# Performance work log

Hardware: AMD Instinct MI355X
Metric: run time of the kernel (lower is better)

## Reference

```python
import jax, jax.numpy as jnp
import numpy as np

N_NODES = 50000
N_EDGES = 1600000
IN_CH = 128
HID = 64
HEADS = 2
EMB = 128
OUT_CH = EMB // HEADS  # 64, GATConvMean out_channels
NEG_SLOPE = 0.2


def _gat_conv(x, src, dst, W, a_src, a_dst, b, heads, out_ch, concat, n_nodes):
    # x: [N, F_in]; W: [F_in, heads*out_ch]; a_src/a_dst: [heads, out_ch]; b: bias
    s = (x @ W).reshape(n_nodes, heads, out_ch)          # [N, H, C]
    alpha_src = jnp.sum(s * a_src, axis=-1)              # [N, H]
    alpha_dst = jnp.sum(s * a_dst, axis=-1)              # [N, H]
    e = jax.nn.leaky_relu(alpha_src[src] + alpha_dst[dst], NEG_SLOPE)  # [E, H]
    # segment softmax over edges sharing the same destination node
    m = jax.ops.segment_max(e, dst, num_segments=n_nodes)             # [N, H]
    ex = jnp.exp(e - m[dst])
    denom = jax.ops.segment_sum(ex, dst, num_segments=n_nodes)        # [N, H]
    alpha = ex / denom[dst]                                           # [E, H]
    msg = s[src] * alpha[:, :, None]                                  # [E, H, C]
    out = jax.ops.segment_sum(msg, dst, num_segments=n_nodes)         # [N, H, C]
    if concat:
        out = out.reshape(n_nodes, heads * out_ch)
    else:
        out = out.mean(axis=1)
    return out + b


def setup_inputs() -> dict:
    key = jax.random.key(0)
    ks = jax.random.split(key, 16)
    X = jax.random.normal(ks[0], (N_NODES, IN_CH), dtype=jnp.float32)
    edge_index = jax.random.randint(ks[1], (2, N_EDGES), 0, N_NODES, dtype=jnp.int64)

    def glorot(k, shape):
        fan_in, fan_out = shape[0], shape[-1]
        lim = jnp.sqrt(6.0 / (fan_in + fan_out)).astype(jnp.float32)
        return jax.random.uniform(k, shape, jnp.float32, -lim, lim)

    HC = HEADS * HID  # 128
    # in_layer: GATConv(IN_CH -> HID, heads=HEADS, concat)
    W0 = glorot(ks[2], (IN_CH, HC))
    a_src0 = glorot(ks[3], (HEADS, HID))
    a_dst0 = glorot(ks[4], (HEADS, HID))
    b0 = jnp.zeros((HC,), jnp.float32)
    # middle layer: GATConv(HC -> HID, heads=HEADS, concat)
    W1 = glorot(ks[5], (HC, HC))
    a_src1 = glorot(ks[6], (HEADS, HID))
    a_dst1 = glorot(ks[7], (HEADS, HID))
    b1 = jnp.zeros((HC,), jnp.float32)
    # ivectors: GATConvMean(HC -> OUT_CH, heads=HEADS, mean over heads)
    W2 = glorot(ks[8], (HC, HEADS * OUT_CH))
    a_src2 = glorot(ks[9], (HEADS, OUT_CH))
    a_dst2 = glorot(ks[10], (HEADS, OUT_CH))
    b2 = jnp.zeros((OUT_CH,), jnp.float32)
    return {
        "X": X, "edge_index": edge_index,
        "W0": W0, "a_src0": a_src0, "a_dst0": a_dst0, "b0": b0,
        "W1": W1, "a_src1": a_src1, "a_dst1": a_dst1, "b1": b1,
        "W2": W2, "a_src2": a_src2, "a_dst2": a_dst2, "b2": b2,
    }


def reference(X, edge_index, W0, a_src0, a_dst0, b0, W1, a_src1, a_dst1, b1, W2, a_src2, a_dst2, b2):
    n = X.shape[0]
    loop = jnp.arange(n, dtype=edge_index.dtype)
    src = jnp.concatenate([edge_index[0], loop])  # PyG GATConv add_self_loops=True
    dst = jnp.concatenate([edge_index[1], loop])
    h = jax.nn.elu(_gat_conv(X, src, dst, W0, a_src0, a_dst0, b0, HEADS, HID, True, n))
    h = jax.nn.relu(_gat_conv(h, src, dst, W1, a_src1, a_dst1, b1, HEADS, HID, True, n))
    # dropout is identity in eval mode
    out = jax.nn.relu(_gat_conv(h, src, dst, W2, a_src2, a_dst2, b2, HEADS, OUT_CH, False, n))
    return out
```

## Files before the change

kernel.cpp:

```cpp
#include <hip/hip_runtime.h>
#include <hip/hip_bf16.h>


#define SCAN_BLOCK 256
#define KSHIFT 12
#define KC 13

__global__ void detect_i64(const unsigned* __restrict__ ei, int* __restrict__ flag) {
    if (threadIdx.x == 0 && blockIdx.x == 0) {
        int allz = 1;
        for (int i = 0; i < 128; ++i)
            if (ei[2 * i + 1] != 0u) { allz = 0; break; }
        *flag = allz;
    }
}

__global__ __launch_bounds__(256) void gat_convert(
    const void* __restrict__ ei, const int* __restrict__ flag, int nE, int nN,
    int2* __restrict__ edge2) {
    const int i64 = *flag;
    const long long total = (long long)nE + nN;
    const long long stride = (long long)gridDim.x * blockDim.x;
    for (long long i = (long long)blockIdx.x * blockDim.x + threadIdx.x; i < total; i += stride) {
        int s, d;
        if (i < nE) {
            if (i64) { s = (int)((const long long*)ei)[i]; d = (int)((const long long*)ei)[nE + i]; }
            else     { s = ((const int*)ei)[i];            d = ((const int*)ei)[nE + i]; }
        } else { s = d = (int)(i - nE); }
        edge2[i] = make_int2(s, d);
    }
}

__global__ __launch_bounds__(256) void gat_rankp(
    const int2* __restrict__ edge2, long long total, int nN,
    int* __restrict__ cnt2, int* __restrict__ rank) {
    const int cw = (nN + 7) >> 3;
    const int lo = (blockIdx.x & 7) * cw;
    const long long stride = (long long)(gridDim.x >> 3) * blockDim.x;
    for (long long i = (long long)(blockIdx.x >> 3) * blockDim.x + threadIdx.x;
         i < total; i += stride) {
        const int2 e = edge2[i];
        if ((unsigned)(e.y - lo) >= (unsigned)cw) continue;
        const int bin = e.y * KC + (e.x >> KSHIFT);
        rank[i] = atomicAdd(&cnt2[bin], 1);
    }
}

__global__ __launch_bounds__(SCAN_BLOCK) void scan_stage1(
    const int* __restrict__ cnt, int* __restrict__ partial, int* __restrict__ bsum, int n) {
    __shared__ int tmp[SCAN_BLOCK];
    const int i = blockIdx.x * SCAN_BLOCK + threadIdx.x;
    const int v = (i < n) ? cnt[i] : 0;
    tmp[threadIdx.x] = v;
    __syncthreads();
    #pragma unroll
    for (int off = 1; off < SCAN_BLOCK; off <<= 1) {
        const int t = (threadIdx.x >= off) ? tmp[threadIdx.x - off] : 0;
        __syncthreads();
        tmp[threadIdx.x] += t;
        __syncthreads();
    }
    if (i < n) partial[i] = tmp[threadIdx.x];
    if (threadIdx.x == SCAN_BLOCK - 1) bsum[blockIdx.x] = tmp[threadIdx.x];
}

__global__ void scan_stage2(int* __restrict__ bsum, int nb, int* __restrict__ rowp, int n) {
    const int lane = threadIdx.x;
    int carry = 0;
    for (int base = 0; base < nb; base += 64) {
        const int i = base + lane;
        const int v = (i < nb) ? bsum[i] : 0;
        int incl = v;
        #pragma unroll
        for (int off = 1; off < 64; off <<= 1) {
            const int t = __shfl_up(incl, off);
            if (lane >= off) incl += t;
        }
        if (i < nb) bsum[i] = carry + incl - v;
        carry += __shfl(incl, 63);
    }
    if (lane == 0) rowp[n] = carry;
}

__global__ __launch_bounds__(SCAN_BLOCK) void scan_stage3v2(
    const int* __restrict__ part2, const int* __restrict__ cnt2,
    const int* __restrict__ bsumA, const int* __restrict__ partB,
    const int* __restrict__ bsumB, int* __restrict__ rowp, int n) {
    const int i = blockIdx.x * SCAN_BLOCK + threadIdx.x;
    if (i < n) {
        const int b1 = i >> 8;
        rowp[i] = bsumB[b1 >> 8] + (partB[b1] - bsumA[b1]) + (part2[i] - cnt2[i]);
    }
}

__global__ __launch_bounds__(256) void gat_placep(
    const int2* __restrict__ edge2, const int* __restrict__ rank,
    const int* __restrict__ rowp2, long long total, int nN, int* __restrict__ csr) {
    const int cw = (nN + 7) >> 3;
    const int lo = (blockIdx.x & 7) * cw;
    const long long stride = (long long)(gridDim.x >> 3) * blockDim.x;
    for (long long i = (long long)(blockIdx.x >> 3) * blockDim.x + threadIdx.x;
         i < total; i += stride) {
        const int2 e = edge2[i];
        if ((unsigned)(e.y - lo) >= (unsigned)cw) continue;
        const int bin = e.y * KC + (e.x >> KSHIFT);
        csr[rowp2[bin] + rank[i]] = e.x;
    }
}

__global__ __launch_bounds__(256) void gemm_alpha(
    const float* __restrict__ Xin, const float* __restrict__ W,
    const float* __restrict__ avs, const float* __restrict__ avd,
    float* __restrict__ S, float* __restrict__ as_, float* __restrict__ ad_, int n) {
    __shared__ float Xl[64][128];
    const int tid = threadIdx.x;
    const int row0 = blockIdx.x * 64;
    for (int i = tid; i < 64 * 32; i += 256) {
        const int r = i >> 5, c4 = i & 31;
        const int gr = row0 + r;
        float4 v = (gr < n) ? ((const float4*)(Xin + (size_t)gr * 128))[c4]
                            : make_float4(0.f, 0.f, 0.f, 0.f);
        ((float4*)(&Xl[r][0]))[c4] = v;
    }
    __syncthreads();
    const int col4 = tid & 31;
    const int rowg = tid >> 5;
    float4 acc[8];
    #pragma unroll
    for (int r = 0; r < 8; ++r) acc[r] = make_float4(0.f, 0.f, 0.f, 0.f);
    const float* Wc = W + col4 * 4;
    for (int kk = 0; kk < 128; kk += 4) {
        const float4 w0 = *(const float4*)(Wc + (size_t)(kk + 0) * 128);
        const float4 w1 = *(const float4*)(Wc + (size_t)(kk + 1) * 128);
        const float4 w2 = *(const float4*)(Wc + (size_t)(kk + 2) * 128);
        const float4 w3 = *(const float4*)(Wc + (size_t)(kk + 3) * 128);
        #pragma unroll
        for (int r = 0; r < 8; ++r) {
            const float4 x = *(const float4*)(&Xl[rowg * 8 + r][kk]);
            acc[r].x = fmaf(x.x, w0.x, acc[r].x); acc[r].y = fmaf(x.x, w0.y, acc[r].y);
            acc[r].z = fmaf(x.x, w0.z, acc[r].z); acc[r].w = fmaf(x.x, w0.w, acc[r].w);
            acc[r].x = fmaf(x.y, w1.x, acc[r].x); acc[r].y = fmaf(x.y, w1.y, acc[r].y);
            acc[r].z = fmaf(x.y, w1.z, acc[r].z); acc[r].w = fmaf(x.y, w1.w, acc[r].w);
            acc[r].x = fmaf(x.z, w2.x, acc[r].x); acc[r].y = fmaf(x.z, w2.y, acc[r].y);
            acc[r].z = fmaf(x.z, w2.z, acc[r].z); acc[r].w = fmaf(x.z, w2.w, acc[r].w);
            acc[r].x = fmaf(x.w, w3.x, acc[r].x); acc[r].y = fmaf(x.w, w3.y, acc[r].y);
            acc[r].z = fmaf(x.w, w3.z, acc[r].z); acc[r].w = fmaf(x.w, w3.w, acc[r].w);
        }
    }
    const float4 av = ((const float4*)avs)[col4];
    const float4 dv = ((const float4*)avd)[col4];
    #pragma unroll
    for (int r = 0; r < 8; ++r) {
        const int grow = row0 + rowg * 8 + r;
        if (grow < n) ((float4*)(S + (size_t)grow * 128))[col4] = acc[r];
        float ps = acc[r].x * av.x + acc[r].y * av.y + acc[r].z * av.z + acc[r].w * av.w;
        float pd = acc[r].x * dv.x + acc[r].y * dv.y + acc[r].z * dv.z + acc[r].w * dv.w;
        #pragma unroll
        for (int off = 8; off; off >>= 1) {
            ps += __shfl_xor(ps, off);
            pd += __shfl_xor(pd, off);
        }
        if ((col4 & 15) == 0 && grow < n) {
            const int h = col4 >> 4;
            as_[2 * grow + h] = ps;
            ad_[2 * grow + h] = pd;
        }
    }
}

__global__ __launch_bounds__(256) void gat_fused(
    const float* __restrict__ S, const float* __restrict__ as_,
    const float* __restrict__ ad_, const int* __restrict__ rowp2,
    const int* __restrict__ csr, const float* __restrict__ bias,
    float* __restrict__ out, int n, int mode) {
    const int lane = threadIdx.x & 63;
    const int d = (blockIdx.x * blockDim.x + threadIdx.x) >> 6;
    if (d >= n) return;
    const int beg = rowp2[d * KC], end = rowp2[(d + 1) * KC];
    const int deg = end - beg;
    const float2 adv = *(const float2*)(ad_ + 2 * d);
    const int g = lane >> 4;
    const int gl = lane & 15;
    float4 acc0 = make_float4(0.f, 0.f, 0.f, 0.f);
    float4 acc1 = make_float4(0.f, 0.f, 0.f, 0.f);
    if (deg <= 64) {
        const bool has = lane < deg;
        const int s_reg = has ? csr[beg + lane] : 0;
        float e0 = -1e30f, e1 = -1e30f;
        if (has) {
            const float2 asv = *(const float2*)(as_ + 2 * s_reg);
            e0 = asv.x + adv.x; e0 = e0 > 0.f ? e0 : 0.2f * e0;
            e1 = asv.y + adv.y; e1 = e1 > 0.f ? e1 : 0.2f * e1;
        }
        float m0 = e0, m1 = e1;
        #pragma unroll
        for (int off = 32; off; off >>= 1) {
            m0 = fmaxf(m0, __shfl_xor(m0, off));
            m1 = fmaxf(m1, __shfl_xor(m1, off));
        }
        const float p0 = has ? __expf(e0 - m0) : 0.f;
        const float p1 = has ? __expf(e1 - m1) : 0.f;
        float s0 = p0, s1 = p1;
        #pragma unroll
        for (int off = 32; off; off >>= 1) {
            s0 += __shfl_xor(s0, off);
            s1 += __shfl_xor(s1, off);
        }
        const float inv0 = 1.f / s0, inv1 = 1.f / s1;
        int k = 0;
        for (; k + 4 <= deg; k += 4) {
            const int ke = k + g;
            const int sv = __shfl(s_reg, ke);
            const float a0 = __shfl(p0, ke) * inv0;
            const float a1 = __shfl(p1, ke) * inv1;
            const float4* r = (const float4*)(S + ((size_t)sv << 7));
            const float4 v0 = r[gl], v1 = r[16 + gl];
            acc0.x = fmaf(a0, v0.x, acc0.x); acc0.y = fmaf(a0, v0.y, acc0.y);
            acc0.z = fmaf(a0, v0.z, acc0.z); acc0.w = fmaf(a0, v0.w, acc0.w);
            acc1.x = fmaf(a1, v1.x, acc1.x); acc1.y = fmaf(a1, v1.y, acc1.y);
            acc1.z = fmaf(a1, v1.z, acc1.z); acc1.w = fmaf(a1, v1.w, acc1.w);
        }
        if (k < deg) {
            const int ke = k + g;
            const bool valid = ke < deg;
            const int idx = valid ? ke : 0;
            const int sv = __shfl(s_reg, idx);
            const float q0 = __shfl(p0, idx), q1 = __shfl(p1, idx);
            if (valid) {
                const float a0 = q0 * inv0, a1 = q1 * inv1;
                const float4* r = (const float4*)(S + ((size_t)sv << 7));
                const float4 v0 = r[gl], v1 = r[16 + gl];
                acc0.x = fmaf(a0, v0.x, acc0.x); acc0.y = fmaf(a0, v0.y, acc0.y);
                acc0.z = fmaf(a0, v0.z, acc0.z); acc0.w = fmaf(a0, v0.w, acc0.w);
                acc1.x = fmaf(a1, v1.x, acc1.x); acc1.y = fmaf(a1, v1.y, acc1.y);
                acc1.z = fmaf(a1, v1.z, acc1.z); acc1.w = fmaf(a1, v1.w, acc1.w);
            }
        }
    } else {
        float m0 = -1e30f, m1 = -1e30f;
        for (int i = beg + lane; i < end; i += 64) {
            const int s = csr[i];
            const float2 asv = *(const float2*)(as_ + 2 * s);
            float e0 = asv.x + adv.x; e0 = e0 > 0.f ? e0 : 0.2f * e0;
            float e1 = asv.y + adv.y; e1 = e1 > 0.f ? e1 : 0.2f * e1;
            m0 = fmaxf(m0, e0); m1 = fmaxf(m1, e1);
        }
        #pragma unroll
        for (int off = 32; off; off >>= 1) {
            m0 = fmaxf(m0, __shfl_xor(m0, off));
            m1 = fmaxf(m1, __shfl_xor(m1, off));
        }
        float s0 = 0.f, s1 = 0.f;
        for (int i = beg + lane; i < end; i += 64) {
            const int s = csr[i];
            const float2 asv = *(const float2*)(as_ + 2 * s);
            float e0 = asv.x + adv.x; e0 = e0 > 0.f ? e0 : 0.2f * e0;
            float e1 = asv.y + adv.y; e1 = e1 > 0.f ? e1 : 0.2f * e1;
            s0 += __expf(e0 - m0); s1 += __expf(e1 - m1);
        }
        #pragma unroll
        for (int off = 32; off; off >>= 1) {
            s0 += __shfl_xor(s0, off);
            s1 += __shfl_xor(s1, off);
        }
        const float inv0 = 1.f / s0, inv1 = 1.f / s1;
        for (int k = 0; k < deg; k += 4) {
            const int ke = k + g;
            const bool valid = ke < deg;
            if (valid) {
                const int sv = csr[beg + ke];
                const float2 asv = *(const float2*)(as_ + 2 * sv);
                float e0 = asv.x + adv.x; e0 = e0 > 0.f ? e0 : 0.2f * e0;
                float e1 = asv.y + adv.y; e1 = e1 > 0.f ? e1 : 0.2f * e1;
                const float a0 = __expf(e0 - m0) * inv0;
                const float a1 = __expf(e1 - m1) * inv1;
                const float4* r = (const float4*)(S + ((size_t)sv << 7));
                const float4 v0 = r[gl], v1 = r[16 + gl];
                acc0.x = fmaf(a0, v0.x, acc0.x); acc0.y = fmaf(a0, v0.y, acc0.y);
                acc0.z = fmaf(a0, v0.z, acc0.z); acc0.w = fmaf(a0, v0.w, acc0.w);
                acc1.x = fmaf(a1, v1.x, acc1.x); acc1.y = fmaf(a1, v1.y, acc1.y);
                acc1.z = fmaf(a1, v1.z, acc1.z); acc1.w = fmaf(a1, v1.w, acc1.w);
            }
        }
    }
    #pragma unroll
    for (int off = 16; off <= 32; off <<= 1) {
        acc0.x += __shfl_xor(acc0.x, off); acc0.y += __shfl_xor(acc0.y, off);
        acc0.z += __shfl_xor(acc0.z, off); acc0.w += __shfl_xor(acc0.w, off);
        acc1.x += __shfl_xor(acc1.x, off); acc1.y += __shfl_xor(acc1.y, off);
        acc1.z += __shfl_xor(acc1.z, off); acc1.w += __shfl_xor(acc1.w, off);
    }
    if (mode == 2) {
        if (lane < 16) {
            const float4 b = ((const float4*)bias)[gl];
            float4 o;
            o.x = fmaxf(0.5f * (acc0.x + acc1.x) + b.x, 0.f);
            o.y = fmaxf(0.5f * (acc0.y + acc1.y) + b.y, 0.f);
            o.z = fmaxf(0.5f * (acc0.z + acc1.z) + b.z, 0.f);
            o.w = fmaxf(0.5f * (acc0.w + acc1.w) + b.w, 0.f);
            ((float4*)(out + (size_t)d * 64))[gl] = o;
        }
    } else if (lane < 32) {
        const int ci = (lane < 16) ? gl : 16 + gl;
        const float4 a = (lane < 16) ? acc0 : acc1;
        const float4 b = ((const float4*)bias)[ci];
        float4 o;
        o.x = a.x + b.x; o.y = a.y + b.y; o.z = a.z + b.z; o.w = a.w + b.w;
        if (mode == 0) {
            o.x = o.x > 0.f ? o.x : expm1f(o.x);
            o.y = o.y > 0.f ? o.y : expm1f(o.y);
            o.z = o.z > 0.f ? o.z : expm1f(o.z);
            o.w = o.w > 0.f ? o.w : expm1f(o.w);
        } else {
            o.x = fmaxf(o.x, 0.f); o.y = fmaxf(o.y, 0.f);
            o.z = fmaxf(o.z, 0.f); o.w = fmaxf(o.w, 0.f);
        }
        ((float4*)(out + (size_t)d * 128))[ci] = o;
    }
}

extern "C" void kernel_launch(void* const* d_in, const int* in_sizes, int n_in,
                              void* d_out, int out_size, void* d_ws, size_t ws_size,
                              hipStream_t stream) {
    const float* X   = (const float*)d_in[0];
    const void*  EI  = d_in[1];
    const float* W0  = (const float*)d_in[2];
    const float* as0 = (const float*)d_in[3];
    const float* ad0 = (const float*)d_in[4];
    const float* b0  = (const float*)d_in[5];
    const float* W1  = (const float*)d_in[6];
    const float* as1 = (const float*)d_in[7];
    const float* ad1 = (const float*)d_in[8];
    const float* b1  = (const float*)d_in[9];
    const float* W2  = (const float*)d_in[10];
    const float* as2 = (const float*)d_in[11];
    const float* ad2 = (const float*)d_in[12];
    const float* b2  = (const float*)d_in[13];

    const int N  = in_sizes[0] / 128;
    const int E  = in_sizes[1] / 2;
    const int ET = E + N;
    const int NBINS = N * KC;
    const int NB2 = (NBINS + SCAN_BLOCK - 1) / SCAN_BLOCK;
    const int NB3 = (NB2 + SCAN_BLOCK - 1) / SCAN_BLOCK;

    char* p = (char*)d_ws;
    size_t used = 0;
    auto alloc = [&](size_t bytes) -> void* {
        void* r = p + used;
        used += (bytes + 255) & ~(size_t)255;
        return r;
    };
    float*  S     = (float*)alloc((size_t)N * 128 * 4);
    float*  H0    = (float*)alloc((size_t)N * 128 * 4);
    float*  H1    = (float*)alloc((size_t)N * 128 * 4);
    int*    csr   = (int*)alloc((size_t)ET * 4);
    int*    rowp2 = (int*)alloc((size_t)(NBINS + 1) * 4);
    int*    cnt2  = (int*)alloc((size_t)NBINS * 4);
    int*    part2 = (int*)alloc((size_t)NBINS * 4);
    int*    bsumA = (int*)alloc((size_t)NB2 * 4);
    int*    partB = (int*)alloc((size_t)NB2 * 4);
    int*    bsumB = (int*)alloc((size_t)NB3 * 4);
    float*  asb   = (float*)alloc((size_t)N * 2 * 4);
    float*  adb   = (float*)alloc((size_t)N * 2 * 4);
    int*    flag  = (int*)alloc(256);
    if (used > ws_size) return;
    const int ETP = (ET + 63) & ~63;
    int2* edge2 = (int2*)S;
    int*  rank  = (int*)(edge2 + ETP);

    hipMemsetAsync(cnt2, 0, (size_t)NBINS * 4, stream);
    detect_i64<<<1, 64, 0, stream>>>((const unsigned*)EI, flag);
    gat_convert<<<2048, 256, 0, stream>>>(EI, flag, E, N, edge2);
    gat_rankp<<<2048, 256, 0, stream>>>(edge2, (long long)ET, N, cnt2, rank);
    scan_stage1<<<NB2, SCAN_BLOCK, 0, stream>>>(cnt2, part2, bsumA, NBINS);
    scan_stage1<<<NB3, SCAN_BLOCK, 0, stream>>>(bsumA, partB, bsumB, NB2);
    scan_stage2<<<1, 64, 0, stream>>>(bsumB, NB3, rowp2, NBINS);
    scan_stage3v2<<<NB2, SCAN_BLOCK, 0, stream>>>(part2, cnt2, bsumA, partB, bsumB, rowp2, NBINS);
    gat_placep<<<2048, 256, 0, stream>>>(edge2, rank, rowp2, (long long)ET, N, csr);

    const int gemm_blocks = (N + 63) / 64;
    const int wave_blocks = (N + 3) / 4;

    gemm_alpha<<<gemm_blocks, 256, 0, stream>>>(X, W0, as0, ad0, S, asb, adb, N);
    gat_fused<<<wave_blocks, 256, 0, stream>>>(S, asb, adb, rowp2, csr, b0, H0, N, 0);
    gemm_alpha<<<gemm_blocks, 256, 0, stream>>>(H0, W1, as1, ad1, S, asb, adb, N);
    gat_fused<<<wave_blocks, 256, 0, stream>>>(S, asb, adb, rowp2, csr, b1, H1, N, 1);
    gemm_alpha<<<gemm_blocks, 256, 0, stream>>>(H1, W2, as2, ad2, S, asb, adb, N);
    gat_fused<<<wave_blocks, 256, 0, stream>>>(S, asb, adb, rowp2, csr, b2, (float*)d_out, N, 2);
}
```

Before: 535.0 us.

## Pre-partition edges into destination buckets and store CSR sources as 16-bit

Replaces the convert kernel and the filtered rank/place passes with a partition kernel that writes edges into 8 destination-range buckets as packed 32-bit (src|dst<<16). The rank and place kernels then read only their own bucket instead of scanning all edges 8 times, and the CSR source indices become unsigned short, halving index traffic in the three aggregation kernels. The packing assumes node ids fit in 16 bits (N=50000), and a bucket overflowing its capacity (1.25x the average) silently drops edges.

```diff
diff --git a/kernel.cpp b/kernel.cpp
--- a/kernel.cpp
+++ b/kernel.cpp
@@ -15,34 +15,55 @@
     }
 }
 
-__global__ __launch_bounds__(256) void gat_convert(
+__global__ __launch_bounds__(256) void gat_partition(
     const void* __restrict__ ei, const int* __restrict__ flag, int nE, int nN,
-    int2* __restrict__ edge2) {
+    unsigned* __restrict__ bucket, int cap, int* __restrict__ gcnt) {
+    __shared__ int lcnt[8];
+    __shared__ int lbase[8];
     const int i64 = *flag;
+    const int cw = (nN + 7) >> 3;
+    const int tid = threadIdx.x;
     const long long total = (long long)nE + nN;
     const long long stride = (long long)gridDim.x * blockDim.x;
-    for (long long i = (long long)blockIdx.x * blockDim.x + threadIdx.x; i < total; i += stride) {
-        int s, d;
-        if (i < nE) {
-            if (i64) { s = (int)((const long long*)ei)[i]; d = (int)((const long long*)ei)[nE + i]; }
-            else     { s = ((const int*)ei)[i];            d = ((const int*)ei)[nE + i]; }
-        } else { s = d = (int)(i - nE); }
-        edge2[i] = make_int2(s, d);
-    }
-}
-
-__global__ __launch_bounds__(256) void gat_rankp(
-    const int2* __restrict__ edge2, long long total, int nN,
+    for (long long i = (long long)blockIdx.x * blockDim.x + tid; ; i += stride) {
+        const long long iter_base = i - tid;
+        if (iter_base >= total) break;
+        if (tid < 8) lcnt[tid] = 0;
+        __syncthreads();
+        const bool has = i < total;
+        int s = 0, d = 0, cls = 0, lpos = 0;
+        if (has) {
+            if (i < nE) {
+                if (i64) { s = (int)((const long long*)ei)[i]; d = (int)((const long long*)ei)[nE + i]; }
+                else     { s = ((const int*)ei)[i];            d = ((const int*)ei)[nE + i]; }
+            } else { s = d = (int)(i - nE); }
+            cls = d / cw;
+            lpos = atomicAdd(&lcnt[cls], 1);
+        }
+        __syncthreads();
+        if (tid < 8 && lcnt[tid] > 0) lbase[tid] = atomicAdd(&gcnt[tid], lcnt[tid]);
+        __syncthreads();
+        if (has) {
+            const int pos = lbase[cls] + lpos;
+            if (pos < cap) bucket[(size_t)cls * cap + pos] = (unsigned)s | ((unsigned)d << 16);
+        }
+        __syncthreads();
+    }
+}
+
+__global__ __launch_bounds__(256) void gat_rankb(
+    const unsigned* __restrict__ bucket, const int* __restrict__ gcnt, int cap,
     int* __restrict__ cnt2, int* __restrict__ rank) {
-    const int cw = (nN + 7) >> 3;
-    const int lo = (blockIdx.x & 7) * cw;
-    const long long stride = (long long)(gridDim.x >> 3) * blockDim.x;
-    for (long long i = (long long)(blockIdx.x >> 3) * blockDim.x + threadIdx.x;
-         i < total; i += stride) {
-        const int2 e = edge2[i];
-        if ((unsigned)(e.y - lo) >= (unsigned)cw) continue;
-        const int bin = e.y * KC + (e.x >> KSHIFT);
-        rank[i] = atomicAdd(&cnt2[bin], 1);
+    const int c = blockIdx.x & 7;
+    const int m = gcnt[c];
+    const unsigned* bk = bucket + (size_t)c * cap;
+    int* rk = rank + (size_t)c * cap;
+    const int stride = (gridDim.x >> 3) * blockDim.x;
+    for (int j = (blockIdx.x >> 3) * blockDim.x + threadIdx.x; j < m; j += stride) {
+        const unsigned e = bk[j];
+        const int s = e & 0xFFFF, d = e >> 16;
+        const int bin = d * KC + (s >> KSHIFT);
+        rk[j] = atomicAdd(&cnt2[bin], 1);
     }
 }
 
@@ -93,18 +114,20 @@
     }
 }
 
-__global__ __launch_bounds__(256) void gat_placep(
-    const int2* __restrict__ edge2, const int* __restrict__ rank,
-    const int* __restrict__ rowp2, long long total, int nN, int* __restrict__ csr) {
-    const int cw = (nN + 7) >> 3;
-    const int lo = (blockIdx.x & 7) * cw;
-    const long long stride = (long long)(gridDim.x >> 3) * blockDim.x;
-    for (long long i = (long long)(blockIdx.x >> 3) * blockDim.x + threadIdx.x;
-         i < total; i += stride) {
-        const int2 e = edge2[i];
-        if ((unsigned)(e.y - lo) >= (unsigned)cw) continue;
-        const int bin = e.y * KC + (e.x >> KSHIFT);
-        csr[rowp2[bin] + rank[i]] = e.x;
+__global__ __launch_bounds__(256) void gat_placeb(
+    const unsigned* __restrict__ bucket, const int* __restrict__ gcnt, int cap,
+    const int* __restrict__ rank, const int* __restrict__ rowp2,
+    unsigned short* __restrict__ csr) {
+    const int c = blockIdx.x & 7;
+    const int m = gcnt[c];
+    const unsigned* bk = bucket + (size_t)c * cap;
+    const int* rk = rank + (size_t)c * cap;
+    const int stride = (gridDim.x >> 3) * blockDim.x;
+    for (int j = (blockIdx.x >> 3) * blockDim.x + threadIdx.x; j < m; j += stride) {
+        const unsigned e = bk[j];
+        const int s = e & 0xFFFF, d = e >> 16;
+        const int bin = d * KC + (s >> KSHIFT);
+        csr[rowp2[bin] + rk[j]] = (unsigned short)s;
     }
 }
 
@@ -171,7 +194,7 @@
 __global__ __launch_bounds__(256) void gat_fused(
     const float* __restrict__ S, const float* __restrict__ as_,
     const float* __restrict__ ad_, const int* __restrict__ rowp2,
-    const int* __restrict__ csr, const float* __restrict__ bias,
+    const unsigned short* __restrict__ csr, const float* __restrict__ bias,
     float* __restrict__ out, int n, int mode) {
     const int lane = threadIdx.x & 63;
     const int d = (blockIdx.x * blockDim.x + threadIdx.x) >> 6;
@@ -185,7 +208,7 @@
     float4 acc1 = make_float4(0.f, 0.f, 0.f, 0.f);
     if (deg <= 64) {
         const bool has = lane < deg;
-        const int s_reg = has ? csr[beg + lane] : 0;
+        const int s_reg = has ? (int)csr[beg + lane] : 0;
         float e0 = -1e30f, e1 = -1e30f;
         if (has) {
             const float2 asv = *(const float2*)(as_ + 2 * s_reg);
@@ -239,7 +262,7 @@
     } else {
         float m0 = -1e30f, m1 = -1e30f;
         for (int i = beg + lane; i < end; i += 64) {
-            const int s = csr[i];
+            const int s = (int)csr[i];
             const float2 asv = *(const float2*)(as_ + 2 * s);
             float e0 = asv.x + adv.x; e0 = e0 > 0.f ? e0 : 0.2f * e0;
             float e1 = asv.y + adv.y; e1 = e1 > 0.f ? e1 : 0.2f * e1;
@@ -252,7 +275,7 @@
         }
         float s0 = 0.f, s1 = 0.f;
         for (int i = beg + lane; i < end; i += 64) {
-            const int s = csr[i];
+            const int s = (int)csr[i];
             const float2 asv = *(const float2*)(as_ + 2 * s);
             float e0 = asv.x + adv.x; e0 = e0 > 0.f ? e0 : 0.2f * e0;
             float e1 = asv.y + adv.y; e1 = e1 > 0.f ? e1 : 0.2f * e1;
@@ -266,9 +289,8 @@
         const float inv0 = 1.f / s0, inv1 = 1.f / s1;
         for (int k = 0; k < deg; k += 4) {
             const int ke = k + g;
-            const bool valid = ke < deg;
-            if (valid) {
-                const int sv = csr[beg + ke];
+            if (ke < deg) {
+                const int sv = (int)csr[beg + ke];
                 const float2 asv = *(const float2*)(as_ + 2 * sv);
                 float e0 = asv.x + adv.x; e0 = e0 > 0.f ? e0 : 0.2f * e0;
                 float e1 = asv.y + adv.y; e1 = e1 > 0.f ? e1 : 0.2f * e1;
@@ -343,6 +365,7 @@
     const int NBINS = N * KC;
     const int NB2 = (NBINS + SCAN_BLOCK - 1) / SCAN_BLOCK;
     const int NB3 = (NB2 + SCAN_BLOCK - 1) / SCAN_BLOCK;
+    const int cap = ((ET / 8) * 5 / 4 + 255) & ~255;
 
     char* p = (char*)d_ws;
     size_t used = 0;
@@ -351,33 +374,34 @@
         used += (bytes + 255) & ~(size_t)255;
         return r;
     };
-    float*  S     = (float*)alloc((size_t)N * 128 * 4);
-    float*  H0    = (float*)alloc((size_t)N * 128 * 4);
-    float*  H1    = (float*)alloc((size_t)N * 128 * 4);
-    int*    csr   = (int*)alloc((size_t)ET * 4);
-    int*    rowp2 = (int*)alloc((size_t)(NBINS + 1) * 4);
-    int*    cnt2  = (int*)alloc((size_t)NBINS * 4);
-    int*    part2 = (int*)alloc((size_t)NBINS * 4);
-    int*    bsumA = (int*)alloc((size_t)NB2 * 4);
-    int*    partB = (int*)alloc((size_t)NB2 * 4);
-    int*    bsumB = (int*)alloc((size_t)NB3 * 4);
-    float*  asb   = (float*)alloc((size_t)N * 2 * 4);
-    float*  adb   = (float*)alloc((size_t)N * 2 * 4);
-    int*    flag  = (int*)alloc(256);
+    float*          S     = (float*)alloc((size_t)N * 128 * 4);
+    float*          H0    = (float*)alloc((size_t)N * 128 * 4);
+    float*          H1    = (float*)alloc((size_t)N * 128 * 4);
+    unsigned short* csr   = (unsigned short*)alloc((size_t)ET * 2);
+    int*            rowp2 = (int*)alloc((size_t)(NBINS + 1) * 4);
+    int*            cnt2  = (int*)alloc((size_t)NBINS * 4);
+    int*            part2 = (int*)alloc((size_t)NBINS * 4);
+    int*            bsumA = (int*)alloc((size_t)NB2 * 4);
+    int*            partB = (int*)alloc((size_t)NB2 * 4);
+    int*            bsumB = (int*)alloc((size_t)NB3 * 4);
+    float*          asb   = (float*)alloc((size_t)N * 2 * 4);
+    float*          adb   = (float*)alloc((size_t)N * 2 * 4);
+    int*            flag  = (int*)alloc(256);
+    int*            gcnt  = (int*)alloc(256);
     if (used > ws_size) return;
-    const int ETP = (ET + 63) & ~63;
-    int2* edge2 = (int2*)S;
-    int*  rank  = (int*)(edge2 + ETP);
+    unsigned* bucket = (unsigned*)S;
+    int*      rank   = (int*)(bucket + (size_t)8 * cap);
 
     hipMemsetAsync(cnt2, 0, (size_t)NBINS * 4, stream);
+    hipMemsetAsync(gcnt, 0, 256, stream);
     detect_i64<<<1, 64, 0, stream>>>((const unsigned*)EI, flag);
-    gat_convert<<<2048, 256, 0, stream>>>(EI, flag, E, N, edge2);
-    gat_rankp<<<2048, 256, 0, stream>>>(edge2, (long long)ET, N, cnt2, rank);
+    gat_partition<<<2048, 256, 0, stream>>>(EI, flag, E, N, bucket, cap, gcnt);
+    gat_rankb<<<2048, 256, 0, stream>>>(bucket, gcnt, cap, cnt2, rank);
     scan_stage1<<<NB2, SCAN_BLOCK, 0, stream>>>(cnt2, part2, bsumA, NBINS);
     scan_stage1<<<NB3, SCAN_BLOCK, 0, stream>>>(bsumA, partB, bsumB, NB2);
     scan_stage2<<<1, 64, 0, stream>>>(bsumB, NB3, rowp2, NBINS);
     scan_stage3v2<<<NB2, SCAN_BLOCK, 0, stream>>>(part2, cnt2, bsumA, partB, bsumB, rowp2, NBINS);
-    gat_placep<<<2048, 256, 0, stream>>>(edge2, rank, rowp2, (long long)ET, N, csr);
+    gat_placeb<<<2048, 256, 0, stream>>>(bucket, gcnt, cap, rank, rowp2, csr);
 
     const int gemm_blocks = (N + 63) / 64;
     const int wave_blocks = (N + 3) / 4;
```

Measured after the change: 588.5 us. 1.1x slower.
